# Performance work log

Hardware: AMD Instinct MI355X
Metric: run time of the kernel (lower is better)

The kernel has to match this reference:

```python
import jax, jax.numpy as jnp
import numpy as np

B, N, CIN, COUT = 16, 4096, 64, 128
M = N // 4          # number of FPS centroids
K = 64              # max_group_size
RADIUS = 0.2
EPS = 1e-5          # BatchNorm eps
BIG = 1e10


def fps(xyz, m):
    # xyz: [N,3] -> m farthest-point-sampled indices (first index = 0)
    n = xyz.shape[0]
    def step(carry, _):
        dists, last = carry
        d = jnp.sum((xyz - xyz[last]) ** 2, axis=-1)
        dists = jnp.minimum(dists, d)
        return (dists, jnp.argmax(dists).astype(jnp.int32)), last
    _, idx = jax.lax.scan(step, (jnp.full((n,), BIG, xyz.dtype), jnp.int32(0)), None, length=m)
    return idx


def ball_query(cent, xyz, radius, k):
    # cent: [M,3], xyz: [N,3] -> [M,K] indices; first-k-within-radius, padded with first hit
    n = xyz.shape[0]
    d2 = jnp.sum((cent[:, None, :] - xyz[None, :, :]) ** 2, axis=-1)  # [M,N]
    within = d2 <= radius * radius
    ar = jnp.arange(n, dtype=jnp.int32)
    key = jnp.where(within, ar, ar + n)         # in-radius points sort first, in index order
    order = jnp.argsort(key, axis=-1)[:, :k]    # first K candidates
    valid = jnp.take_along_axis(within, order, axis=-1)
    return jnp.where(valid, order, order[:, :1])


def conv1x1(x, w, b):
    # x: [B,C,K,M], w: [O,C] (Conv2d 1x1)
    return jnp.einsum('bckm,oc->bokm', x, w) + b[None, :, None, None]


def bnorm(x, g, b):
    # BatchNorm2d training-mode forward: stats over (B,K,M)
    mu = jnp.mean(x, axis=(0, 2, 3), keepdims=True)
    var = jnp.var(x, axis=(0, 2, 3), keepdims=True)
    return g[None, :, None, None] * (x - mu) * jax.lax.rsqrt(var + EPS) + b[None, :, None, None]


def setup_inputs() -> dict:
    key = jax.random.key(0)
    ks = jax.random.split(key, 6)
    def xavier(k, o, i):
        lim = float(np.sqrt(6.0 / (o + i)))
        return jax.random.uniform(k, (o, i), jnp.float32, -lim, lim)
    return {
        'points': jax.random.uniform(ks[0], (B, 3, N), jnp.float32),
        'point_features': jax.random.normal(ks[1], (B, CIN, N), jnp.float32),
        'w1': xavier(ks[2], CIN, CIN + 3), 'b1': jnp.zeros((CIN,), jnp.float32),
        'g1': jnp.ones((CIN,), jnp.float32), 'beta1': jnp.zeros((CIN,), jnp.float32),
        'w2': xavier(ks[3], CIN, CIN), 'b2': jnp.zeros((CIN,), jnp.float32),
        'g2': jnp.ones((CIN,), jnp.float32), 'beta2': jnp.zeros((CIN,), jnp.float32),
        'w3': xavier(ks[4], COUT, CIN), 'b3': jnp.zeros((COUT,), jnp.float32),
    }


def reference(points, point_features, w1, b1, g1, beta1, w2, b2, g2, beta2, w3, b3):
    xyz = jnp.transpose(points, (0, 2, 1))            # [B,N,3]
    feats = jnp.transpose(point_features, (0, 2, 1))  # [B,N,CIN]
    fps_idx = jax.vmap(lambda p: fps(p, M))(xyz)      # [B,M]
    cent = jax.vmap(lambda p, i: p[i])(xyz, fps_idx)  # [B,M,3]
    gidx = jax.vmap(lambda c, p: ball_query(c, p, RADIUS, K))(cent, xyz)  # [B,M,K]
    gxyz = jax.vmap(lambda p, i: p[i])(xyz, gidx) - cent[:, :, None, :]   # [B,M,K,3] relative coords
    gfeat = jax.vmap(lambda f, i: f[i])(feats, gidx)                      # [B,M,K,CIN]
    regions = jnp.concatenate([gxyz, gfeat], axis=-1)                     # [B,M,K,CIN+3]
    x = jnp.transpose(regions, (0, 3, 2, 1))                              # [B,CIN+3,K,M]
    x = jax.nn.relu(bnorm(conv1x1(x, w1, b1), g1, beta1))
    x = jax.nn.relu(bnorm(conv1x1(x, w2, b2), g2, beta2))
    x = conv1x1(x, w3, b3)
    centroid_features = jnp.max(x, axis=2)             # max over group dim -> [B,COUT,M]
    centroids = cent.reshape(B, 3, M)                  # faithful to original .view(B, 3, -1)
    return centroids, centroid_features
```

## Files before the change

kernel.cpp:

```cpp
#include <hip/hip_runtime.h>

#define NB   16
#define NPT  4096
#define CINF 64
#define COUTF 128
#define MC   1024
#define KG   64
#define PTOT (NB*KG*MC)

typedef unsigned short u16;
typedef unsigned int   u32;
typedef unsigned long long u64;

static __device__ __forceinline__ float blv(u16 v){ return __uint_as_float(((u32)v) << 16); }
static __device__ __forceinline__ u16 f2b(float f){
  u32 x = __float_as_uint(f);
  return (u16)((x + 0x7fffu + ((x >> 16) & 1u)) >> 16);
}

template<bool BF> struct io;
template<> struct io<true>{
  static __device__ __forceinline__ float ld(const void* p, size_t i){ return blv(((const u16*)p)[i]); }
  static __device__ __forceinline__ void st(void* p, size_t i, float v){ ((u16*)p)[i] = f2b(v); }
};
template<> struct io<false>{
  static __device__ __forceinline__ float ld(const void* p, size_t i){ return ((const float*)p)[i]; }
  static __device__ __forceinline__ void st(void* p, size_t i, float v){ ((float*)p)[i] = v; }
};

template<bool BF>
static __device__ __forceinline__ float4 ldw4(const void* w, int idx){
  if constexpr (BF) {
    ushort4 u = *(const ushort4*)((const u16*)w + idx);
    return make_float4(blv(u.x), blv(u.y), blv(u.z), blv(u.w));
  } else return *(const float4*)((const float*)w + idx);
}
template<bool BF>
static __device__ __forceinline__ void ldw8(const void* w, int idx, float4& a, float4& b){
  if constexpr (BF) {
    ushort4 u0 = *(const ushort4*)((const u16*)w + idx);
    ushort4 u1 = *(const ushort4*)((const u16*)w + idx + 4);
    a = make_float4(blv(u0.x), blv(u0.y), blv(u0.z), blv(u0.w));
    b = make_float4(blv(u1.x), blv(u1.y), blv(u1.z), blv(u1.w));
  } else {
    a = *(const float4*)((const float*)w + idx);
    b = *(const float4*)((const float*)w + idx + 4);
  }
}

__global__ __launch_bounds__(256) void detect_kernel(const void* pts, int* flagp, double* dstats)
{
  const int t = threadIdx.x;
  if (t < 64) {
    u32 w = ((const u32*)pts)[t];
    u64 m = __ballot((w & 0xFFFFu) < 0x4000u);
    if (t == 0) *flagp = (m == ~0ull) ? 1 : 0;
  }
  dstats[t] = 0.0;
}

template<bool BF>
static __device__ void fps_body(const void* pts, float* __restrict__ centw, void* out,
                                float* smp)
{
  float* lx = smp; float* ly = smp + NPT; float* lz = smp + 2*NPT;
  u64 (*red)[4] = (u64(*)[4])(smp + 3*NPT);
  const int t = threadIdx.x, b = blockIdx.x;
  const size_t pbase = (size_t)b*3*NPT;
  for (int i = t; i < NPT; i += 256) {
    lx[i] = io<BF>::ld(pts, pbase + i);
    ly[i] = io<BF>::ld(pts, pbase + NPT + i);
    lz[i] = io<BF>::ld(pts, pbase + 2*NPT + i);
  }
  __syncthreads();
  float qx[16],qy[16],qz[16],dd[16];
  const int base = t*16;
  #pragma unroll
  for (int j=0;j<16;++j){ qx[j]=lx[base+j]; qy[j]=ly[base+j]; qz[j]=lz[base+j]; dd[j]=1e10f; }
  int last = 0;
  const int lane = t & 63, wv = t >> 6;
  for (int it = 0; it < MC; ++it) {
    float cx = lx[last], cy = ly[last], cz = lz[last];
    if (t < 3) {
      float v = (t==0)?cx:((t==1)?cy:cz);
      centw[((size_t)b*MC + it)*3 + t] = v;
      io<BF>::st(out, (size_t)b*3*MC + (size_t)it*3 + t, v);
    }
    float bv = -1.f; int bi = base;
    #pragma unroll
    for (int j=0;j<16;++j) {
      float dx = __fsub_rn(qx[j], cx);
      float dy = __fsub_rn(qy[j], cy);
      float dz = __fsub_rn(qz[j], cz);
      float d  = __fadd_rn(__fadd_rn(__fmul_rn(dx,dx), __fmul_rn(dy,dy)), __fmul_rn(dz,dz));
      float nd = fminf(dd[j], d);
      dd[j] = nd;
      if (nd > bv) { bv = nd; bi = base + j; }
    }
    float mv = bv;
    #pragma unroll
    for (int off = 1; off < 64; off <<= 1) mv = fmaxf(mv, __shfl_xor(mv, off, 64));
    u64 wm = __ballot(bv == mv);
    int fl = __ffsll((long long)wm) - 1;
    int wbi = __shfl(bi, fl, 64);
    if (lane == 0) red[it & 1][wv] = ((u64)__float_as_uint(mv) << 32) | (u32)(~wbi);
    __syncthreads();
    u64 k0 = red[it&1][0], k1 = red[it&1][1];
    u64 k2 = red[it&1][2], k3 = red[it&1][3];
    if (k1 > k0) k0 = k1;
    if (k3 > k2) k2 = k3;
    if (k2 > k0) k0 = k2;
    last = (int)(~(u32)k0);
  }
}

template<bool BF>
static __device__ void g1_body(const void* pts, const void* feats, const void* w1p,
                               float* __restrict__ G1, float* smp)
{
  float* Xs = smp;
  void*  w1sh = (void*)(smp + 4352);
  const int idx = blockIdx.x - NB;
  const int b = idx >> 6;
  const int n0 = (idx & 63) * 64;
  const int t = threadIdx.x, lane = t & 63, wv = t >> 6;
  for (int e = t; e < 4352; e += 256) {
    int cp = e >> 6, co = e & 63;
    int src = (cp < 64) ? (co*67 + cp + 3) : (cp < 67 ? co*67 + cp - 64 : -1);
    if constexpr (BF) ((u16*)w1sh)[e]   = (src >= 0) ? ((const u16*)w1p)[src]   : (u16)0;
    else              ((float*)w1sh)[e] = (src >= 0) ? ((const float*)w1p)[src] : 0.f;
  }
  {
    float* xrow = Xs + lane*68;
    const size_t fb = ((size_t)b*CINF)*NPT + n0 + lane;
    #pragma unroll
    for (int j = 0; j < 16; ++j) {
      int c = wv*16 + j;
      xrow[c] = io<BF>::ld(feats, fb + (size_t)c*NPT);
    }
    if (wv == 0) {
      const size_t pb = (size_t)b*3*NPT + n0 + lane;
      xrow[64] = io<BF>::ld(pts, pb);
      xrow[65] = io<BF>::ld(pts, pb + NPT);
      xrow[66] = io<BF>::ld(pts, pb + 2*NPT);
      xrow[67] = 0.f;
    }
  }
  __syncthreads();
  const int kq = lane >> 4, coq = lane & 15;
  const int co0 = coq*4, k0 = wv*16 + kq*4;
  float acc[4][4];
  #pragma unroll
  for (int r=0;r<4;++r){
    #pragma unroll
    for (int j=0;j<4;++j) acc[r][j] = 0.f;
  }
  {
    const float* xb = Xs + (size_t)k0*68;
    for (int c4 = 0; c4 < 17; ++c4) {
      float4 xv[4], wr[4];
      #pragma unroll
      for (int r=0;r<4;++r) xv[r] = *(const float4*)(xb + r*68 + c4*4);
      #pragma unroll
      for (int q=0;q<4;++q) wr[q] = ldw4<BF>(w1sh, (c4*4+q)*64 + co0);
      #pragma unroll
      for (int q=0;q<4;++q){
        const float* w = (const float*)&wr[q];
        #pragma unroll
        for (int r=0;r<4;++r){
          const float x = ((const float*)&xv[r])[q];
          #pragma unroll
          for (int j=0;j<4;++j) acc[r][j] = fmaf(x, w[j], acc[r][j]);
        }
      }
    }
  }
  #pragma unroll
  for (int r=0;r<4;++r)
    *(float4*)(G1 + ((size_t)b*NPT + n0 + k0 + r)*64 + co0)
      = make_float4(acc[r][0],acc[r][1],acc[r][2],acc[r][3]);
}

__global__ __launch_bounds__(256) void fps_tr_kernel(const void* pts, const void* feats,
    const void* w1p, float* centw, float* G1, void* out, const int* flagp)
{
  __shared__ alignas(16) float smp[3*NPT + 16];
  if (blockIdx.x < NB) {
    if (*flagp) fps_body<true >(pts, centw, out, smp);
    else        fps_body<false>(pts, centw, out, smp);
  } else {
    if (*flagp) g1_body<true >(pts, feats, w1p, G1, smp);
    else        g1_body<false>(pts, feats, w1p, G1, smp);
  }
}

template<bool BF>
static __device__ void ballq_body(const void* pts, const float* __restrict__ centw,
                                  int* __restrict__ gidx)
{
  const int lane = threadIdx.x & 63;
  const int g = blockIdx.x*4 + (threadIdx.x >> 6);
  const int b = g >> 10;
  const size_t pbase = (size_t)b*3*NPT;
  const float cx = centw[(size_t)g*3+0], cy = centw[(size_t)g*3+1], cz = centw[(size_t)g*3+2];
  int* gout = gidx + (size_t)g*KG;
  int taken = 0, idx0 = 0;
  for (int s = 0; s < NPT; s += 64) {
    int n = s + lane;
    float dx = __fsub_rn(cx, io<BF>::ld(pts, pbase + n));
    float dy = __fsub_rn(cy, io<BF>::ld(pts, pbase + NPT + n));
    float dz = __fsub_rn(cz, io<BF>::ld(pts, pbase + 2*NPT + n));
    float d2 = __fadd_rn(__fadd_rn(__fmul_rn(dx,dx), __fmul_rn(dy,dy)), __fmul_rn(dz,dz));
    u64 mask = __ballot(d2 <= 0.04f);
    if (mask) {
      if (taken == 0) idx0 = s + __ffsll((long long)mask) - 1;
      bool win = (mask >> lane) & 1;
      int pos = taken + __popcll(mask & ((1ull << lane) - 1ull));
      if (win && pos < KG) gout[pos] = n;
      taken += (int)__popcll(mask);
      if (taken >= KG) break;
    }
  }
  int cnt = taken < KG ? taken : KG;
  if (lane >= cnt) gout[lane] = idx0;
}

__global__ __launch_bounds__(256) void ballq_kernel(const void* pts, const float* centw,
                                                    int* gidx, const int* flagp)
{
  if (*flagp) ballq_body<true >(pts, centw, gidx);
  else        ballq_body<false>(pts, centw, gidx);
}


template<bool BF>
__global__ __launch_bounds__(256) void p1_kernel(
    const void* w1p, const void* b1p,
    const float* __restrict__ centw, const int* __restrict__ gidxp,
    const float* __restrict__ G1,
    double* __restrict__ dstats, const int* __restrict__ flagp)
{
  if ((*flagp != 0) != BF) return;
  __shared__ int gids[64];
  __shared__ float d1s[64];
  __shared__ float w1cs[192];
  __shared__ float b1s[64];
  __shared__ float sbuf[128];
  const int t = threadIdx.x, lane = t & 63, cq = t >> 6;
  if (t < 64) {
    w1cs[t*3+0] = io<BF>::ld(w1p, (size_t)t*67 + 0);
    w1cs[t*3+1] = io<BF>::ld(w1p, (size_t)t*67 + 1);
    w1cs[t*3+2] = io<BF>::ld(w1p, (size_t)t*67 + 2);
    b1s[t] = io<BF>::ld(b1p, t);
  }
  const int g0 = blockIdx.x * 32;
  const int b = g0 >> 10;
  float s16[16], q16[16];
  #pragma unroll
  for (int j=0;j<16;++j){ s16[j]=0.f; q16[j]=0.f; }
  __syncthreads();
  for (int i = 0; i < 32; ++i) {
    const int g = g0 + i;
    if (t < 64) {
      gids[t] = gidxp[(size_t)g*KG + t];
      float cx = centw[(size_t)g*3], cy = centw[(size_t)g*3+1], cz = centw[(size_t)g*3+2];
      d1s[t] = b1s[t] - (w1cs[t*3]*cx + w1cs[t*3+1]*cy + w1cs[t*3+2]*cz);
    }
    __syncthreads();
    const float* row = G1 + ((size_t)b*NPT + gids[lane])*64 + cq*16;
    float vbuf[16];
    *(float4*)(vbuf)      = ((const float4*)row)[0];
    *(float4*)(vbuf + 4)  = ((const float4*)row)[1];
    *(float4*)(vbuf + 8)  = ((const float4*)row)[2];
    *(float4*)(vbuf + 12) = ((const float4*)row)[3];
    #pragma unroll
    for (int j=0;j<16;++j){
      float a = vbuf[j] + d1s[cq*16+j];
      s16[j] += a; q16[j] = fmaf(a, a, q16[j]);
    }
    __syncthreads();
  }
  #pragma unroll
  for (int j=0;j<16;++j){
    #pragma unroll
    for (int off = 1; off < 64; off <<= 1){
      s16[j] += __shfl_xor(s16[j], off, 64);
      q16[j] += __shfl_xor(q16[j], off, 64);
    }
  }
  if (lane == 0) {
    #pragma unroll
    for (int j=0;j<16;++j){ sbuf[cq*16+j] = s16[j]; sbuf[64+cq*16+j] = q16[j]; }
  }
  __syncthreads();
  if (t < 128) atomicAdd(&dstats[t], (double)sbuf[t]);
}

template<bool BF>
__global__ __launch_bounds__(256) void p2_kernel(
    const void* w1p, const void* b1p, const void* w2p, const void* b2p,
    const float* __restrict__ fstats, double* __restrict__ dstats,
    const float* __restrict__ centw, const int* __restrict__ gidxp,
    const float* __restrict__ G1, const int* __restrict__ flagp)
{
  if ((*flagp != 0) != BF) return;
  __shared__ alignas(16) float z1[2][4352];
  __shared__ alignas(16) unsigned char w2raw[BF ? 4096*2 : 4096*4];
  __shared__ float scsh[128];
  __shared__ int gids[128];
  __shared__ float c3s[6];

  const int t = threadIdx.x, lane = t & 63, wv = t >> 6;
  const int kq = lane >> 4, coq = lane & 15;
  const int co0 = coq * 4;
  const int k0  = wv*16 + kq*4;
  const int b   = blockIdx.x >> 7;
  const int m0  = (blockIdx.x & 127) * 8;
  const int c0  = (t*4) & 63;
  const int srow = t >> 4;

  for (int e = t; e < 4096; e += 256) {
    int src = (e & 63)*64 + (e >> 6);
    if constexpr (BF) ((u16*)w2raw)[e] = ((const u16*)w2p)[src];
    else              ((float*)w2raw)[e] = ((const float*)w2p)[src];
  }
  if (t < 128) scsh[t] = fstats[t];
  float b2v[4], w1c_r[12], b1_r[4];
  #pragma unroll
  for (int j=0;j<4;++j){
    b2v[j] = io<BF>::ld(b2p, co0+j);
    b1_r[j] = io<BF>::ld(b1p, c0+j);
    #pragma unroll
    for (int i=0;i<3;++i) w1c_r[j*3+i] = io<BF>::ld(w1p, (size_t)(c0+j)*67 + i);
  }
  __syncthreads();
  float scr[4], shr[4];
  #pragma unroll
  for (int j=0;j<4;++j){ scr[j] = scsh[c0+j]; shr[j] = scsh[64+c0+j]; }
  float sp[4] = {0,0,0,0}, qp[4] = {0,0,0,0};

  for (int mo = 0; mo < 4; ++mo) {
    const size_t g0 = (size_t)b*MC + m0 + mo*2;
    if (t < 128) gids[t] = gidxp[g0*KG + t];
    if (t < 6)   c3s[t]  = centw[g0*3 + t];
    __syncthreads();
    #pragma unroll
    for (int g=0;g<2;++g){
      float d1[4];
      {
        const float cx = c3s[g*3], cy = c3s[g*3+1], cz = c3s[g*3+2];
        #pragma unroll
        for (int j=0;j<4;++j)
          d1[j] = b1_r[j] - (w1c_r[j*3]*cx + w1c_r[j*3+1]*cy + w1c_r[j*3+2]*cz);
      }
      #pragma unroll
      for (int u=0;u<4;++u){
        const int row = u*16 + srow;
        const int gi = gids[g*64 + row];
        float4 v = *(const float4*)(G1 + ((size_t)b*NPT + gi)*64 + c0);
        float4 z;
        z.x = fmaxf(0.f, fmaf(v.x + d1[0], scr[0], shr[0]));
        z.y = fmaxf(0.f, fmaf(v.y + d1[1], scr[1], shr[1]));
        z.z = fmaxf(0.f, fmaf(v.z + d1[2], scr[2], shr[2]));
        z.w = fmaxf(0.f, fmaf(v.w + d1[3], scr[3], shr[3]));
        *(float4*)(z1[g] + (size_t)row*68 + c0) = z;
      }
    }
    __syncthreads();
    float acc[2][4][4];
    #pragma unroll
    for (int g=0;g<2;++g)
      #pragma unroll
      for (int r=0;r<4;++r)
        #pragma unroll
        for (int j=0;j<4;++j) acc[g][r][j] = b2v[j];
    {
      const float* zb0 = z1[0] + (size_t)k0*68;
      const float* zb1 = z1[1] + (size_t)k0*68;
      for (int c4 = 0; c4 < 16; ++c4) {
        float4 wr[4];
        #pragma unroll
        for (int q=0;q<4;++q) wr[q] = ldw4<BF>(w2raw, (c4*4+q)*64 + co0);
        float4 xv[2][4];
        #pragma unroll
        for (int r=0;r<4;++r){ xv[0][r] = *(const float4*)(zb0 + r*68 + c4*4);
                               xv[1][r] = *(const float4*)(zb1 + r*68 + c4*4); }
        #pragma unroll
        for (int q=0;q<4;++q){
          const float* w = (const float*)&wr[q];
          #pragma unroll
          for (int g=0;g<2;++g)
            #pragma unroll
            for (int r=0;r<4;++r){
              const float x = ((const float*)&xv[g][r])[q];
              #pragma unroll
              for (int j=0;j<4;++j) acc[g][r][j] = fmaf(x, w[j], acc[g][r][j]);
            }
        }
      }
    }
    #pragma unroll
    for (int g=0;g<2;++g){
      #pragma unroll
      for (int j=0;j<4;++j){
        sp[j] += (acc[g][0][j]+acc[g][1][j]) + (acc[g][2][j]+acc[g][3][j]);
        qp[j]  = fmaf(acc[g][0][j],acc[g][0][j], fmaf(acc[g][1][j],acc[g][1][j],
                 fmaf(acc[g][2][j],acc[g][2][j], fmaf(acc[g][3][j],acc[g][3][j], qp[j]))));
      }
    }
    __syncthreads();
  }
  float* sbuf = z1[0];
  #pragma unroll
  for (int j=0;j<4;++j){ sbuf[t*4+j] = sp[j]; sbuf[1024 + t*4+j] = qp[j]; }
  __syncthreads();
  if (t < 64) {
    const int cq = t >> 2, jj = t & 3;
    float s=0.f, q=0.f;
    #pragma unroll
    for (int i=0;i<16;++i){
      const int tp = cq + 16*i;
      s += sbuf[tp*4 + jj];
      q += sbuf[1024 + tp*4 + jj];
    }
    atomicAdd(&dstats[128 + t], (double)s);
    atomicAdd(&dstats[192 + t], (double)q);
  }
}

template<bool BF>
__global__ __launch_bounds__(256) void p3_kernel(
    const void* w1p, const void* b1p, const void* w2p, const void* b2p,
    const void* w3p, const void* b3p,
    const float* __restrict__ fstats,
    const float* __restrict__ centw, const int* __restrict__ gidxp,
    const float* __restrict__ G1, void* out, const int* __restrict__ flagp)
{
  if ((*flagp != 0) != BF) return;
  __shared__ alignas(16) float z[4352];
  __shared__ alignas(16) unsigned char w2raw[BF ? 4096*2 : 4096*4];
  __shared__ alignas(16) unsigned char w3raw[BF ? 8192*2 : 8192*4];
  __shared__ float scsh[256];
  __shared__ int gids[64];
  __shared__ float c3s[3];

  const int t = threadIdx.x, lane = t & 63, wv = t >> 6;
  const int kq = lane >> 4, coq = lane & 15;
  const int co0 = coq * 4;
  const int co08 = coq * 8;
  const int k0  = wv*16 + kq*4;
  const int b   = blockIdx.x >> 7;
  const int m0  = (blockIdx.x & 127) * 8;
  const int c0  = (t*4) & 63;
  const int srow = t >> 4;

  for (int e = t; e < 4096; e += 256) {
    int src = (e & 63)*64 + (e >> 6);
    if constexpr (BF) ((u16*)w2raw)[e] = ((const u16*)w2p)[src];
    else              ((float*)w2raw)[e] = ((const float*)w2p)[src];
  }
  for (int e = t; e < 8192; e += 256) {
    int src = (e & 127)*64 + (e >> 7);
    if constexpr (BF) ((u16*)w3raw)[e] = ((const u16*)w3p)[src];
    else              ((float*)w3raw)[e] = ((const float*)w3p)[src];
  }
  scsh[t] = fstats[t];
  float b2v[4], b3v[8], w1c_r[12], b1_r[4];
  #pragma unroll
  for (int j=0;j<4;++j){
    b2v[j] = io<BF>::ld(b2p, co0+j);
    b1_r[j] = io<BF>::ld(b1p, c0+j);
    #pragma unroll
    for (int i=0;i<3;++i) w1c_r[j*3+i] = io<BF>::ld(w1p, (size_t)(c0+j)*67 + i);
  }
  #pragma unroll
  for (int j=0;j<8;++j) b3v[j] = io<BF>::ld(b3p, co08+j);
  __syncthreads();
  float scr[4], shr[4], sc2[4], sh2[4];
  #pragma unroll
  for (int j=0;j<4;++j){
    scr[j] = scsh[c0+j];  shr[j] = scsh[64+c0+j];
    sc2[j] = scsh[128+co0+j]; sh2[j] = scsh[192+co0+j];
  }
  float outv[8];

  for (int mi = 0; mi < 8; ++mi) {
    const size_t g = (size_t)b*MC + m0 + mi;
    if (t < 64) gids[t] = gidxp[g*KG + t];
    if (t < 3)  c3s[t]  = centw[g*3 + t];
    __syncthreads();
    {
      float d1[4];
      const float cx = c3s[0], cy = c3s[1], cz = c3s[2];
      #pragma unroll
      for (int j=0;j<4;++j)
        d1[j] = b1_r[j] - (w1c_r[j*3]*cx + w1c_r[j*3+1]*cy + w1c_r[j*3+2]*cz);
      #pragma unroll
      for (int u=0;u<4;++u){
        const int row = u*16 + srow;
        const int gi = gids[row];
        float4 v = *(const float4*)(G1 + ((size_t)b*NPT + gi)*64 + c0);
        float4 zz;
        zz.x = fmaxf(0.f, fmaf(v.x + d1[0], scr[0], shr[0]));
        zz.y = fmaxf(0.f, fmaf(v.y + d1[1], scr[1], shr[1]));
        zz.z = fmaxf(0.f, fmaf(v.z + d1[2], scr[2], shr[2]));
        zz.w = fmaxf(0.f, fmaf(v.w + d1[3], scr[3], shr[3]));
        *(float4*)(z + (size_t)row*68 + c0) = zz;
      }
    }
    __syncthreads();
    float acc2[4][4];
    #pragma unroll
    for (int r=0;r<4;++r){
      #pragma unroll
      for (int j=0;j<4;++j) acc2[r][j] = b2v[j];
    }
    {
      const float* zb = z + (size_t)k0*68;
      for (int c4 = 0; c4 < 16; ++c4) {
        float4 xv[4], wr[4];
        #pragma unroll
        for (int r=0;r<4;++r) xv[r] = *(const float4*)(zb + r*68 + c4*4);
        #pragma unroll
        for (int q=0;q<4;++q) wr[q] = ldw4<BF>(w2raw, (c4*4+q)*64 + co0);
        #pragma unroll
        for (int q=0;q<4;++q){
          const float* w = (const float*)&wr[q];
          #pragma unroll
          for (int r=0;r<4;++r){
            const float x = ((const float*)&xv[r])[q];
            #pragma unroll
            for (int j=0;j<4;++j) acc2[r][j] = fmaf(x, w[j], acc2[r][j]);
          }
        }
      }
    }
    __syncthreads();
    #pragma unroll
    for (int r=0;r<4;++r){
      float4 zv;
      zv.x = fmaxf(0.f, fmaf(acc2[r][0], sc2[0], sh2[0]));
      zv.y = fmaxf(0.f, fmaf(acc2[r][1], sc2[1], sh2[1]));
      zv.z = fmaxf(0.f, fmaf(acc2[r][2], sc2[2], sh2[2]));
      zv.w = fmaxf(0.f, fmaf(acc2[r][3], sc2[3], sh2[3]));
      *(float4*)(z + (size_t)(k0+r)*68 + co0) = zv;
    }
    __syncthreads();
    float a3[4][8];
    #pragma unroll
    for (int r=0;r<4;++r){
      #pragma unroll
      for (int j=0;j<8;++j) a3[r][j] = b3v[j];
    }
    {
      const float* zb = z + (size_t)k0*68;
      for (int c4 = 0; c4 < 16; ++c4) {
        float4 xv[4], wr[4][2];
        #pragma unroll
        for (int r=0;r<4;++r) xv[r] = *(const float4*)(zb + r*68 + c4*4);
        #pragma unroll
        for (int q=0;q<4;++q) ldw8<BF>(w3raw, (c4*4+q)*128 + co08, wr[q][0], wr[q][1]);
        #pragma unroll
        for (int q=0;q<4;++q){
          const float* w = (const float*)&wr[q][0];
          #pragma unroll
          for (int r=0;r<4;++r){
            const float x = ((const float*)&xv[r])[q];
            #pragma unroll
            for (int j=0;j<8;++j) a3[r][j] = fmaf(x, w[j], a3[r][j]);
          }
        }
      }
    }
    __syncthreads();
    float* redm = z;
    #pragma unroll
    for (int j=0;j<8;++j){
      float mv = fmaxf(fmaxf(a3[0][j],a3[1][j]), fmaxf(a3[2][j],a3[3][j]));
      redm[(co08+j)*17 + wv*4 + kq] = mv;
    }
    __syncthreads();
    if (t < 128) {
      const float* rr = redm + t*17;
      float s = rr[0];
      #pragma unroll
      for (int i=1;i<16;++i) s = fmaxf(s, rr[i]);
      outv[mi] = s;
    }
    __syncthreads();
  }
  if (t < 128) {
    const size_t obase = (size_t)NB*3*MC + ((size_t)b*COUTF + t)*MC + m0;
    if (BF) {
      uint4 v;
      v.x = (u32)f2b(outv[0]) | ((u32)f2b(outv[1]) << 16);
      v.y = (u32)f2b(outv[2]) | ((u32)f2b(outv[3]) << 16);
      v.z = (u32)f2b(outv[4]) | ((u32)f2b(outv[5]) << 16);
      v.w = (u32)f2b(outv[6]) | ((u32)f2b(outv[7]) << 16);
      *(uint4*)((u16*)out + obase) = v;
    } else {
      float* op = (float*)out + obase;
      *(float4*)(op)     = make_float4(outv[0],outv[1],outv[2],outv[3]);
      *(float4*)(op + 4) = make_float4(outv[4],outv[5],outv[6],outv[7]);
    }
  }
}

template<int STAGE, bool BF>
__global__ __launch_bounds__(256) void mlp_kernel(
    const void* pts, const void* feats,
    const void* w1p, const void* b1p, const void* w2p, const void* b2p,
    const void* w3p, const void* b3p,
    const float* __restrict__ centw, const int* __restrict__ gidxp,
    double* __restrict__ dstats, const float* __restrict__ fstats, void* out,
    const int* __restrict__ flagp)
{
  if ((*flagp != 0) != BF) return;
  constexpr int ACTF = 4352 + (STAGE>=2 ? 4352 : 0);
  constexpr int W1B  = BF ? 4352*2 : 4352*4;
  constexpr int W2B  = (STAGE>=2) ? (BF ? 4096*2 : 4096*4) : 0;
  constexpr int W3B  = (STAGE==3) ? (BF ? 8192*2 : 8192*4) : 0;
  constexpr int REDB = (STAGE==1) ? 8704 : 0;
  constexpr int SMB  = ACTF*4 + W1B + W2B + W3B + REDB;
  __shared__ alignas(16) unsigned char smem[SMB];
  __shared__ int gids[64];
  __shared__ float c3s[3];
  float* Xs  = (float*)smem;
  float* z1s = Xs + 4352;
  void*  w1t = smem + ACTF*4;
  void*  w2t = smem + ACTF*4 + W1B;
  void*  w3t = smem + ACTF*4 + W1B + W2B;
  float* red = (STAGE==1) ? (float*)(smem + ACTF*4 + W1B) : z1s;
  const int t = threadIdx.x, lane = t & 63, wv = t >> 6;
  const int kq = lane >> 4, coq = lane & 15;
  const int co0 = coq * 4, co08 = coq * 8;
  const int k0  = wv*16 + kq*4;
  const int b   = blockIdx.x >> 7;
  const int m0  = (blockIdx.x & 127) * 8;
  for (int e = t; e < 4352; e += 256) {
    int cp = e >> 6, co = e & 63;
    int src = (cp < 64) ? (co*67 + cp + 3) : (cp < 67 ? co*67 + cp - 64 : -1);
    if constexpr (BF) ((u16*)w1t)[e]  = (src >= 0) ? ((const u16*)w1p)[src]  : (u16)0;
    else              ((float*)w1t)[e] = (src >= 0) ? ((const float*)w1p)[src] : 0.f;
  }
  if constexpr (STAGE >= 2)
    for (int e = t; e < 4096; e += 256) {
      int src = (e & 63)*64 + (e >> 6);
      if constexpr (BF) ((u16*)w2t)[e] = ((const u16*)w2p)[src];
      else              ((float*)w2t)[e] = ((const float*)w2p)[src];
    }
  if constexpr (STAGE == 3)
    for (int e = t; e < 8192; e += 256) {
      int src = (e & 127)*64 + (e >> 7);
      if constexpr (BF) ((u16*)w3t)[e] = ((const u16*)w3p)[src];
      else              ((float*)w3t)[e] = ((const float*)w3p)[src];
    }
  float b1v[4], b2v[4], sc1v[4], sh1v[4], sc2v[4], sh2v[4], b3v[8];
  #pragma unroll
  for (int j=0;j<4;++j) b1v[j] = io<BF>::ld(b1p, co0+j);
  if constexpr (STAGE >= 2) {
    #pragma unroll
    for (int j=0;j<4;++j) {
      b2v[j]  = io<BF>::ld(b2p, co0+j);
      sc1v[j] = fstats[co0+j]; sh1v[j] = fstats[64+co0+j];
    }
  }
  if constexpr (STAGE == 3) {
    #pragma unroll
    for (int j=0;j<4;++j) { sc2v[j] = fstats[128+co0+j]; sh2v[j] = fstats[192+co0+j]; }
    #pragma unroll
    for (int j=0;j<8;++j) b3v[j] = io<BF>::ld(b3p, co08+j);
  }
  float run_s = 0.f, run_q = 0.f;
  float outv[8];
  __syncthreads();
  for (int mi = 0; mi < 8; ++mi) {
    const int m = m0 + mi;
    const size_t g = (size_t)b*MC + m;
    if (t < 64) gids[t] = gidxp[g*KG + t];
    if (t < 3)  c3s[t]  = centw[g*3 + t];
    __syncthreads();
    {
      const int gi = gids[lane];
      float* xrow = Xs + lane*68;
      const int cs = wv*16;
      for (int c = cs; c < cs+16; ++c)
        xrow[c] = io<BF>::ld(feats, ((size_t)b*CINF + c)*NPT + gi);
      if (wv == 0) {
        const size_t pbase = (size_t)b*3*NPT;
        xrow[64] = __fsub_rn(io<BF>::ld(pts, pbase + gi),         c3s[0]);
        xrow[65] = __fsub_rn(io<BF>::ld(pts, pbase + NPT + gi),   c3s[1]);
        xrow[66] = __fsub_rn(io<BF>::ld(pts, pbase + 2*NPT + gi), c3s[2]);
        xrow[67] = 0.f;
      }
    }
    __syncthreads();
    float acc[4][4];
    #pragma unroll
    for (int r=0;r<4;++r){
      #pragma unroll
      for (int j=0;j<4;++j) acc[r][j] = b1v[j];
    }
    {
      const float* xb = Xs + (size_t)k0*68;
      for (int c4 = 0; c4 < 17; ++c4) {
        float4 xv[4], wr[4];
        #pragma unroll
        for (int r=0;r<4;++r) xv[r] = *(const float4*)(xb + r*68 + c4*4);
        #pragma unroll
        for (int q=0;q<4;++q) wr[q] = ldw4<BF>(w1t, (c4*4+q)*64 + co0);
        #pragma unroll
        for (int q=0;q<4;++q){
          const float* w = (const float*)&wr[q];
          #pragma unroll
          for (int r=0;r<4;++r){
            const float x = ((const float*)&xv[r])[q];
            #pragma unroll
            for (int j=0;j<4;++j) acc[r][j] = fmaf(x, w[j], acc[r][j]);
          }
        }
      }
    }
    if constexpr (STAGE == 1) {
      #pragma unroll
      for (int j=0;j<4;++j){
        float s  = (acc[0][j]+acc[1][j]) + (acc[2][j]+acc[3][j]);
        float q2 = fmaf(acc[0][j],acc[0][j], fmaf(acc[1][j],acc[1][j],
                   fmaf(acc[2][j],acc[2][j], acc[3][j]*acc[3][j])));
        red[(co0+j)*17 + wv*4 + kq] = s;
        red[1088 + (co0+j)*17 + wv*4 + kq] = q2;
      }
      __syncthreads();
      if (t < 64) {
        const float* r1 = red + t*17; const float* r2 = red + 1088 + t*17;
        float s=0.f, q=0.f;
        #pragma unroll
        for (int i=0;i<16;++i){ s += r1[i]; q += r2[i]; }
        run_s += s; run_q += q;
      }
    } else {
      #pragma unroll
      for (int r=0;r<4;++r){
        float4 zv;
        zv.x = fmaxf(0.f, fmaf(acc[r][0], sc1v[0], sh1v[0]));
        zv.y = fmaxf(0.f, fmaf(acc[r][1], sc1v[1], sh1v[1]));
        zv.z = fmaxf(0.f, fmaf(acc[r][2], sc1v[2], sh1v[2]));
        zv.w = fmaxf(0.f, fmaf(acc[r][3], sc1v[3], sh1v[3]));
        *(float4*)(z1s + (size_t)(k0+r)*68 + co0) = zv;
      }
      __syncthreads();
      float acc2[4][4];
      #pragma unroll
      for (int r=0;r<4;++r){
        #pragma unroll
        for (int j=0;j<4;++j) acc2[r][j] = b2v[j];
      }
      {
        const float* zb = z1s + (size_t)k0*68;
        for (int c4 = 0; c4 < 16; ++c4) {
          float4 xv[4], wr[4];
          #pragma unroll
          for (int r=0;r<4;++r) xv[r] = *(const float4*)(zb + r*68 + c4*4);
          #pragma unroll
          for (int q=0;q<4;++q) wr[q] = ldw4<BF>(w2t, (c4*4+q)*64 + co0);
          #pragma unroll
          for (int q=0;q<4;++q){
            const float* w = (const float*)&wr[q];
            #pragma unroll
            for (int r=0;r<4;++r){
              const float x = ((const float*)&xv[r])[q];
              #pragma unroll
              for (int j=0;j<4;++j) acc2[r][j] = fmaf(x, w[j], acc2[r][j]);
            }
          }
        }
      }
      if constexpr (STAGE == 2) {
        __syncthreads();
        #pragma unroll
        for (int j=0;j<4;++j){
          float s  = (acc2[0][j]+acc2[1][j]) + (acc2[2][j]+acc2[3][j]);
          float q2 = fmaf(acc2[0][j],acc2[0][j], fmaf(acc2[1][j],acc2[1][j],
                     fmaf(acc2[2][j],acc2[2][j], acc2[3][j]*acc2[3][j])));
          red[(co0+j)*17 + wv*4 + kq] = s;
          red[1088 + (co0+j)*17 + wv*4 + kq] = q2;
        }
        __syncthreads();
        if (t < 64) {
          const float* r1 = red + t*17; const float* r2 = red + 1088 + t*17;
          float s=0.f, q=0.f;
          #pragma unroll
          for (int i=0;i<16;++i){ s += r1[i]; q += r2[i]; }
          run_s += s; run_q += q;
        }
      } else {
        #pragma unroll
        for (int r=0;r<4;++r){
          float4 zv;
          zv.x = fmaxf(0.f, fmaf(acc2[r][0], sc2v[0], sh2v[0]));
          zv.y = fmaxf(0.f, fmaf(acc2[r][1], sc2v[1], sh2v[1]));
          zv.z = fmaxf(0.f, fmaf(acc2[r][2], sc2v[2], sh2v[2]));
          zv.w = fmaxf(0.f, fmaf(acc2[r][3], sc2v[3], sh2v[3]));
          *(float4*)(Xs + (size_t)(k0+r)*68 + co0) = zv;
        }
        __syncthreads();
        float a3[4][8];
        #pragma unroll
        for (int r=0;r<4;++r){
          #pragma unroll
          for (int j=0;j<8;++j) a3[r][j] = b3v[j];
        }
        {
          const float* zb = Xs + (size_t)k0*68;
          for (int c4 = 0; c4 < 16; ++c4) {
            float4 xv[4], wr[4][2];
            #pragma unroll
            for (int r=0;r<4;++r) xv[r] = *(const float4*)(zb + r*68 + c4*4);
            #pragma unroll
            for (int q=0;q<4;++q) ldw8<BF>(w3t, (c4*4+q)*128 + co08, wr[q][0], wr[q][1]);
            #pragma unroll
            for (int q=0;q<4;++q){
              const float* w = (const float*)&wr[q][0];
              #pragma unroll
              for (int r=0;r<4;++r){
                const float x = ((const float*)&xv[r])[q];
                #pragma unroll
                for (int j=0;j<8;++j) a3[r][j] = fmaf(x, w[j], a3[r][j]);
              }
            }
          }
        }
        float* redm = red;
        #pragma unroll
        for (int j=0;j<8;++j){
          float mv = fmaxf(fmaxf(a3[0][j],a3[1][j]), fmaxf(a3[2][j],a3[3][j]));
          redm[(co08+j)*17 + wv*4 + kq] = mv;
        }
        __syncthreads();
        if (t < 128) {
          const float* rr = redm + t*17;
          float s = rr[0];
          #pragma unroll
          for (int i=1;i<16;++i) s = fmaxf(s, rr[i]);
          outv[mi] = s;
        }
      }
    }
  }
  if constexpr (STAGE <= 2) {
    if (t < 64) {
      atomicAdd(&dstats[(STAGE==1 ? 0 : 128) + lane], (double)run_s);
      atomicAdd(&dstats[(STAGE==1 ? 64 : 192) + lane], (double)run_q);
    }
  } else {
    if (t < 128) {
      const size_t obase = (size_t)NB*3*MC + ((size_t)b*COUTF + t)*MC + m0;
      if (BF) {
        uint4 v;
        v.x = (u32)f2b(outv[0]) | ((u32)f2b(outv[1]) << 16);
        v.y = (u32)f2b(outv[2]) | ((u32)f2b(outv[3]) << 16);
        v.z = (u32)f2b(outv[4]) | ((u32)f2b(outv[5]) << 16);
        v.w = (u32)f2b(outv[6]) | ((u32)f2b(outv[7]) << 16);
        *(uint4*)((u16*)out + obase) = v;
      } else {
        float* op = (float*)out + obase;
        *(float4*)(op)     = make_float4(outv[0],outv[1],outv[2],outv[3]);
        *(float4*)(op + 4) = make_float4(outv[4],outv[5],outv[6],outv[7]);
      }
    }
  }
}

__global__ void finalize_kernel(const double* __restrict__ dstats, float* __restrict__ fstats,
                                const void* g, const void* beta, const int* flagp, int stage)
{
  const int t = threadIdx.x;
  const int off = (stage==1) ? 0 : 128;
  const double inv = 1.0 / (double)PTOT;
  double mu = dstats[off + t] * inv;
  double q  = dstats[off + 64 + t] * inv;
  double var = q - mu*mu;
  if (var < 0.0) var = 0.0;
  float gg, bb;
  if (*flagp) { gg = blv(((const u16*)g)[t]);  bb = blv(((const u16*)beta)[t]); }
  else        { gg = ((const float*)g)[t];     bb = ((const float*)beta)[t]; }
  double scale = (double)gg / sqrt(var + 1e-5);
  fstats[off + t]      = (float)scale;
  fstats[off + 64 + t] = bb - (float)(mu*scale);
}

extern "C" void kernel_launch(void* const* d_in, const int* in_sizes, int n_in,
                              void* d_out, int out_size, void* d_ws, size_t ws_size,
                              hipStream_t stream)
{
  (void)in_sizes; (void)n_in; (void)out_size;
  const void* pts  = d_in[0];
  const void* feats= d_in[1];
  const void* w1   = d_in[2];
  const void* b1   = d_in[3];
  const void* g1   = d_in[4];
  const void* be1  = d_in[5];
  const void* w2   = d_in[6];
  const void* b2   = d_in[7];
  const void* g2   = d_in[8];
  const void* be2  = d_in[9];
  const void* w3   = d_in[10];
  const void* b3   = d_in[11];

  char* ws = (char*)d_ws;
  int*    flag   = (int*)ws;
  double* dstats = (double*)(ws + 64);
  float*  fstats = (float*)(ws + 2112);
  float*  centw  = (float*)(ws + 4096);
  int*    gidx   = (int*)(ws + 200704);
  float*  G1     = (float*)(ws + 4395008);
  const bool gpath = ws_size >= 21172224ull;

  detect_kernel<<<1, 256, 0, stream>>>(pts, flag, dstats);
  fps_tr_kernel<<<gpath ? (NB + NB*NPT/64) : NB, 256, 0, stream>>>(pts, feats, w1, centw, G1, d_out, flag);
  ballq_kernel<<<NB*MC/4, 256, 0, stream>>>(pts, centw, gidx, flag);

  if (gpath) {
    p1_kernel<true ><<<NB*MC/32, 256, 0, stream>>>(w1, b1, centw, gidx, G1, dstats, flag);
    p1_kernel<false><<<NB*MC/32, 256, 0, stream>>>(w1, b1, centw, gidx, G1, dstats, flag);
    finalize_kernel<<<1, 64, 0, stream>>>(dstats, fstats, g1, be1, flag, 1);
    p2_kernel<true ><<<NB*MC/8, 256, 0, stream>>>(w1, b1, w2, b2, fstats, dstats, centw, gidx, G1, flag);
    p2_kernel<false><<<NB*MC/8, 256, 0, stream>>>(w1, b1, w2, b2, fstats, dstats, centw, gidx, G1, flag);
    finalize_kernel<<<1, 64, 0, stream>>>(dstats, fstats, g2, be2, flag, 2);
    p3_kernel<true ><<<NB*MC/8, 256, 0, stream>>>(w1, b1, w2, b2, w3, b3, fstats, centw, gidx, G1, d_out, flag);
    p3_kernel<false><<<NB*MC/8, 256, 0, stream>>>(w1, b1, w2, b2, w3, b3, fstats, centw, gidx, G1, d_out, flag);
  } else {
    const int GRID = NB*MC/8;
    mlp_kernel<1,true ><<<GRID, 256, 0, stream>>>(pts,feats,w1,b1,w2,b2,w3,b3,centw,gidx,dstats,fstats,d_out,flag);
    mlp_kernel<1,false><<<GRID, 256, 0, stream>>>(pts,feats,w1,b1,w2,b2,w3,b3,centw,gidx,dstats,fstats,d_out,flag);
    finalize_kernel<<<1, 64, 0, stream>>>(dstats, fstats, g1, be1, flag, 1);
    mlp_kernel<2,true ><<<GRID, 256, 0, stream>>>(pts,feats,w1,b1,w2,b2,w3,b3,centw,gidx,dstats,fstats,d_out,flag);
    mlp_kernel<2,false><<<GRID, 256, 0, stream>>>(pts,feats,w1,b1,w2,b2,w3,b3,centw,gidx,dstats,fstats,d_out,flag);
    finalize_kernel<<<1, 64, 0, stream>>>(dstats, fstats, g2, be2, flag, 2);
    mlp_kernel<3,true ><<<GRID, 256, 0, stream>>>(pts,feats,w1,b1,w2,b2,w3,b3,centw,gidx,dstats,fstats,d_out,flag);
    mlp_kernel<3,false><<<GRID, 256, 0, stream>>>(pts,feats,w1,b1,w2,b2,w3,b3,centw,gidx,dstats,fstats,d_out,flag);
  }
}
```

Before: 1.396 ms.

## Shorten FPS iteration critical path with DPP reduction and centroid coords in reduction

Replaces the shuffle-xor max reduction in farthest point sampling with DPP row operations plus a readlane, which should have lower latency. The winning point's coordinates now travel with the reduction key through shared memory, so the dependent shared-memory load of the next centroid is gone. Per-iteration global stores of centroids are buffered in LDS and written out once at the end. The cost is more shared memory, which could reduce occupancy for the co-scheduled G1 blocks that share this kernel.

```diff
diff --git a/kernel.cpp b/kernel.cpp
--- a/kernel.cpp
+++ b/kernel.cpp
@@ -48,6 +48,9 @@
   }
 }
 
+#define DPPMAXF(x, ctrl) \
+  (x) = fmaxf((x), __uint_as_float((u32)__builtin_amdgcn_update_dpp(0, (int)__float_as_uint(x), (ctrl), 0xF, 0xF, true)))
+
 __global__ __launch_bounds__(256) void detect_kernel(const void* pts, int* flagp, double* dstats)
 {
   const int t = threadIdx.x;
@@ -64,7 +67,9 @@
                                 float* smp)
 {
   float* lx = smp; float* ly = smp + NPT; float* lz = smp + 2*NPT;
-  u64 (*red)[4] = (u64(*)[4])(smp + 3*NPT);
+  float* cbuf = smp + 3*NPT;
+  u64*   rk   = (u64*)(smp + 3*NPT + 3072);
+  float4* rc  = (float4*)(smp + 3*NPT + 3072 + 16);
   const int t = threadIdx.x, b = blockIdx.x;
   const size_t pbase = (size_t)b*3*NPT;
   for (int i = t; i < NPT; i += 256) {
@@ -77,16 +82,12 @@
   const int base = t*16;
   #pragma unroll
   for (int j=0;j<16;++j){ qx[j]=lx[base+j]; qy[j]=ly[base+j]; qz[j]=lz[base+j]; dd[j]=1e10f; }
-  int last = 0;
   const int lane = t & 63, wv = t >> 6;
+  float cx = lx[0], cy = ly[0], cz = lz[0];
   for (int it = 0; it < MC; ++it) {
-    float cx = lx[last], cy = ly[last], cz = lz[last];
-    if (t < 3) {
-      float v = (t==0)?cx:((t==1)?cy:cz);
-      centw[((size_t)b*MC + it)*3 + t] = v;
-      io<BF>::st(out, (size_t)b*3*MC + (size_t)it*3 + t, v);
-    }
+    if (t == 0) { cbuf[it*3] = cx; cbuf[it*3+1] = cy; cbuf[it*3+2] = cz; }
     float bv = -1.f; int bi = base;
+    float bcx = qx[0], bcy = qy[0], bcz = qz[0];
     #pragma unroll
     for (int j=0;j<16;++j) {
       float dx = __fsub_rn(qx[j], cx);
@@ -95,22 +96,38 @@
       float d  = __fadd_rn(__fadd_rn(__fmul_rn(dx,dx), __fmul_rn(dy,dy)), __fmul_rn(dz,dz));
       float nd = fminf(dd[j], d);
       dd[j] = nd;
-      if (nd > bv) { bv = nd; bi = base + j; }
-    }
-    float mv = bv;
-    #pragma unroll
-    for (int off = 1; off < 64; off <<= 1) mv = fmaxf(mv, __shfl_xor(mv, off, 64));
+      if (nd > bv) { bv = nd; bi = base + j; bcx = qx[j]; bcy = qy[j]; bcz = qz[j]; }
+    }
+    float m = bv;
+    DPPMAXF(m, 0x111);
+    DPPMAXF(m, 0x112);
+    DPPMAXF(m, 0x114);
+    DPPMAXF(m, 0x118);
+    DPPMAXF(m, 0x142);
+    DPPMAXF(m, 0x143);
+    const float mv = __uint_as_float((u32)__builtin_amdgcn_readlane((int)__float_as_uint(m), 63));
     u64 wm = __ballot(bv == mv);
     int fl = __ffsll((long long)wm) - 1;
-    int wbi = __shfl(bi, fl, 64);
-    if (lane == 0) red[it & 1][wv] = ((u64)__float_as_uint(mv) << 32) | (u32)(~wbi);
-    __syncthreads();
-    u64 k0 = red[it&1][0], k1 = red[it&1][1];
-    u64 k2 = red[it&1][2], k3 = red[it&1][3];
-    if (k1 > k0) k0 = k1;
-    if (k3 > k2) k2 = k3;
-    if (k2 > k0) k0 = k2;
-    last = (int)(~(u32)k0);
+    const int p = it & 1;
+    if (lane == fl) {
+      rk[p*4 + wv] = ((u64)__float_as_uint(mv) << 32) | (u32)(~bi);
+      rc[p*4 + wv] = make_float4(bcx, bcy, bcz, 0.f);
+    }
+    __syncthreads();
+    u64 ka = rk[p*4+0], kb = rk[p*4+1], kc2 = rk[p*4+2], kd = rk[p*4+3];
+    float4 c0 = rc[p*4+0], c1 = rc[p*4+1], c2 = rc[p*4+2], c3 = rc[p*4+3];
+    bool s01 = kb > ka;  u64 k01 = s01 ? kb : ka;
+    bool s23 = kd > kc2; u64 k23 = s23 ? kd : kc2;
+    float cwx = s01 ? c1.x : c0.x, cwy = s01 ? c1.y : c0.y, cwz = s01 ? c1.z : c0.z;
+    float cvx = s23 ? c3.x : c2.x, cvy = s23 ? c3.y : c2.y, cvz = s23 ? c3.z : c2.z;
+    bool sx = k23 > k01;
+    cx = sx ? cvx : cwx; cy = sx ? cvy : cwy; cz = sx ? cvz : cwz;
+  }
+  __syncthreads();
+  for (int i = t; i < 3*MC; i += 256) {
+    float v = cbuf[i];
+    centw[(size_t)b*3*MC + i] = v;
+    io<BF>::st(out, (size_t)b*3*MC + i, v);
   }
 }
 
@@ -184,7 +201,7 @@
 __global__ __launch_bounds__(256) void fps_tr_kernel(const void* pts, const void* feats,
     const void* w1p, float* centw, float* G1, void* out, const int* flagp)
 {
-  __shared__ alignas(16) float smp[3*NPT + 16];
+  __shared__ alignas(16) float smp[15408];
   if (blockIdx.x < NB) {
     if (*flagp) fps_body<true >(pts, centw, out, smp);
     else        fps_body<false>(pts, centw, out, smp);
```

Result: slower. 1.497 ms (+7.3%).

## Restructure p3 kernel to per-wave groups with larger register tiles

Applied to the files above, without the earlier changes.

Rewrites the final MLP stage so that each wavefront independently processes its own centroid group in a private shared-memory slice. Each thread now computes an 8x8 (conv2) and 8x16 (conv3) register tile instead of 4x4/4x8, and block-wide __syncthreads are removed from the inner loop. The grid is cut to 512 blocks that handle 32 groups each, and the max reduction is done per wave with direct scattered output stores. This aims to cut barrier overhead and raise arithmetic intensity per LDS load. In exchange it uses much more register pressure and LDS (launch_bounds 256,1), which may reduce occupancy, and the output writes are less coalesced.

```diff
diff --git a/kernel.cpp b/kernel.cpp
--- a/kernel.cpp
+++ b/kernel.cpp
@@ -429,7 +429,7 @@
 }
 
 template<bool BF>
-__global__ __launch_bounds__(256) void p3_kernel(
+__global__ __launch_bounds__(256, 1) void p3_kernel(
     const void* w1p, const void* b1p, const void* w2p, const void* b2p,
     const void* w3p, const void* b3p,
     const float* __restrict__ fstats,
@@ -437,22 +437,17 @@
     const float* __restrict__ G1, void* out, const int* __restrict__ flagp)
 {
   if ((*flagp != 0) != BF) return;
-  __shared__ alignas(16) float z[4352];
+  __shared__ alignas(16) float z[4][4352];
   __shared__ alignas(16) unsigned char w2raw[BF ? 4096*2 : 4096*4];
   __shared__ alignas(16) unsigned char w3raw[BF ? 8192*2 : 8192*4];
-  __shared__ float scsh[256];
-  __shared__ int gids[64];
-  __shared__ float c3s[3];
+  __shared__ alignas(16) float scsh[256];
+  __shared__ alignas(16) float w1cs[192];
+  __shared__ alignas(16) float b1s[64];
+  __shared__ alignas(16) float d1b[4][64];
+  __shared__ alignas(16) float pm[4][1056];
 
   const int t = threadIdx.x, lane = t & 63, wv = t >> 6;
-  const int kq = lane >> 4, coq = lane & 15;
-  const int co0 = coq * 4;
-  const int co08 = coq * 8;
-  const int k0  = wv*16 + kq*4;
-  const int b   = blockIdx.x >> 7;
-  const int m0  = (blockIdx.x & 127) * 8;
-  const int c0  = (t*4) & 63;
-  const int srow = t >> 4;
+  const int lr = lane >> 3, lc = lane & 7;
 
   for (int e = t; e < 4096; e += 256) {
     int src = (e & 63)*64 + (e >> 6);
@@ -465,143 +460,156 @@
     else              ((float*)w3raw)[e] = ((const float*)w3p)[src];
   }
   scsh[t] = fstats[t];
-  float b2v[4], b3v[8], w1c_r[12], b1_r[4];
-  #pragma unroll
-  for (int j=0;j<4;++j){
-    b2v[j] = io<BF>::ld(b2p, co0+j);
-    b1_r[j] = io<BF>::ld(b1p, c0+j);
-    #pragma unroll
-    for (int i=0;i<3;++i) w1c_r[j*3+i] = io<BF>::ld(w1p, (size_t)(c0+j)*67 + i);
-  }
-  #pragma unroll
-  for (int j=0;j<8;++j) b3v[j] = io<BF>::ld(b3p, co08+j);
+  if (t < 64) {
+    w1cs[t*3+0] = io<BF>::ld(w1p, (size_t)t*67 + 0);
+    w1cs[t*3+1] = io<BF>::ld(w1p, (size_t)t*67 + 1);
+    w1cs[t*3+2] = io<BF>::ld(w1p, (size_t)t*67 + 2);
+    b1s[t] = io<BF>::ld(b1p, t);
+  }
+  float b2v[8], b3v[16], sc2r[8], sh2r[8];
+  #pragma unroll
+  for (int j=0;j<8;++j)  b2v[j] = io<BF>::ld(b2p, lc*8 + j);
+  #pragma unroll
+  for (int j=0;j<16;++j) b3v[j] = io<BF>::ld(b3p, lc*16 + j);
   __syncthreads();
-  float scr[4], shr[4], sc2[4], sh2[4];
-  #pragma unroll
-  for (int j=0;j<4;++j){
-    scr[j] = scsh[c0+j];  shr[j] = scsh[64+c0+j];
-    sc2[j] = scsh[128+co0+j]; sh2[j] = scsh[192+co0+j];
-  }
-  float outv[8];
-
-  for (int mi = 0; mi < 8; ++mi) {
-    const size_t g = (size_t)b*MC + m0 + mi;
-    if (t < 64) gids[t] = gidxp[g*KG + t];
-    if (t < 3)  c3s[t]  = centw[g*3 + t];
-    __syncthreads();
+  #pragma unroll
+  for (int j=0;j<8;++j){ sc2r[j] = scsh[128 + lc*8 + j]; sh2r[j] = scsh[192 + lc*8 + j]; }
+
+  float* zw = z[wv];
+  float* pmw = pm[wv];
+
+  for (int gi_it = 0; gi_it < 8; ++gi_it) {
+    const int g = blockIdx.x*32 + wv*8 + gi_it;
+    const int b = g >> 10, m = g & (MC-1);
     {
-      float d1[4];
-      const float cx = c3s[0], cy = c3s[1], cz = c3s[2];
-      #pragma unroll
-      for (int j=0;j<4;++j)
-        d1[j] = b1_r[j] - (w1c_r[j*3]*cx + w1c_r[j*3+1]*cy + w1c_r[j*3+2]*cz);
-      #pragma unroll
-      for (int u=0;u<4;++u){
-        const int row = u*16 + srow;
-        const int gi = gids[row];
-        float4 v = *(const float4*)(G1 + ((size_t)b*NPT + gi)*64 + c0);
+      const float cx = centw[(size_t)g*3], cy = centw[(size_t)g*3+1], cz = centw[(size_t)g*3+2];
+      d1b[wv][lane] = b1s[lane] - (w1cs[lane*3]*cx + w1cs[lane*3+1]*cy + w1cs[lane*3+2]*cz);
+    }
+    {
+      const int gi = gidxp[(size_t)g*KG + lane];
+      const float* grow = G1 + ((size_t)b*NPT + gi)*64;
+      float* zrow = zw + (size_t)lane*68;
+      #pragma unroll
+      for (int c0 = 0; c0 < 64; c0 += 4) {
+        float4 gv = *(const float4*)(grow + c0);
+        float4 dv = *(const float4*)(&d1b[wv][c0]);
+        float4 s1 = *(const float4*)(&scsh[c0]);
+        float4 h1 = *(const float4*)(&scsh[64 + c0]);
         float4 zz;
-        zz.x = fmaxf(0.f, fmaf(v.x + d1[0], scr[0], shr[0]));
-        zz.y = fmaxf(0.f, fmaf(v.y + d1[1], scr[1], shr[1]));
-        zz.z = fmaxf(0.f, fmaf(v.z + d1[2], scr[2], shr[2]));
-        zz.w = fmaxf(0.f, fmaf(v.w + d1[3], scr[3], shr[3]));
-        *(float4*)(z + (size_t)row*68 + c0) = zz;
-      }
-    }
-    __syncthreads();
-    float acc2[4][4];
-    #pragma unroll
-    for (int r=0;r<4;++r){
-      #pragma unroll
-      for (int j=0;j<4;++j) acc2[r][j] = b2v[j];
-    }
+        zz.x = fmaxf(0.f, fmaf(gv.x + dv.x, s1.x, h1.x));
+        zz.y = fmaxf(0.f, fmaf(gv.y + dv.y, s1.y, h1.y));
+        zz.z = fmaxf(0.f, fmaf(gv.z + dv.z, s1.z, h1.z));
+        zz.w = fmaxf(0.f, fmaf(gv.w + dv.w, s1.w, h1.w));
+        *(float4*)(zrow + c0) = zz;
+      }
+    }
+    float acc[8][8];
+    #pragma unroll
+    for (int r=0;r<8;++r)
+      #pragma unroll
+      for (int j=0;j<8;++j) acc[r][j] = b2v[j];
     {
-      const float* zb = z + (size_t)k0*68;
+      const float* zb = zw + (size_t)(lr*8)*68;
       for (int c4 = 0; c4 < 16; ++c4) {
-        float4 xv[4], wr[4];
-        #pragma unroll
-        for (int r=0;r<4;++r) xv[r] = *(const float4*)(zb + r*68 + c4*4);
-        #pragma unroll
-        for (int q=0;q<4;++q) wr[q] = ldw4<BF>(w2raw, (c4*4+q)*64 + co0);
+        float4 xv[8], wA[4], wB[4];
+        #pragma unroll
+        for (int r=0;r<8;++r) xv[r] = *(const float4*)(zb + r*68 + c4*4);
+        #pragma unroll
+        for (int q=0;q<4;++q) ldw8<BF>(w2raw, (c4*4+q)*64 + lc*8, wA[q], wB[q]);
         #pragma unroll
         for (int q=0;q<4;++q){
-          const float* w = (const float*)&wr[q];
-          #pragma unroll
-          for (int r=0;r<4;++r){
+          const float* wa = (const float*)&wA[q];
+          const float* wb = (const float*)&wB[q];
+          #pragma unroll
+          for (int r=0;r<8;++r){
             const float x = ((const float*)&xv[r])[q];
             #pragma unroll
-            for (int j=0;j<4;++j) acc2[r][j] = fmaf(x, w[j], acc2[r][j]);
+            for (int j=0;j<4;++j){
+              acc[r][j]   = fmaf(x, wa[j], acc[r][j]);
+              acc[r][4+j] = fmaf(x, wb[j], acc[r][4+j]);
+            }
           }
         }
       }
     }
-    __syncthreads();
-    #pragma unroll
-    for (int r=0;r<4;++r){
-      float4 zv;
-      zv.x = fmaxf(0.f, fmaf(acc2[r][0], sc2[0], sh2[0]));
-      zv.y = fmaxf(0.f, fmaf(acc2[r][1], sc2[1], sh2[1]));
-      zv.z = fmaxf(0.f, fmaf(acc2[r][2], sc2[2], sh2[2]));
-      zv.w = fmaxf(0.f, fmaf(acc2[r][3], sc2[3], sh2[3]));
-      *(float4*)(z + (size_t)(k0+r)*68 + co0) = zv;
-    }
-    __syncthreads();
-    float a3[4][8];
-    #pragma unroll
-    for (int r=0;r<4;++r){
-      #pragma unroll
-      for (int j=0;j<8;++j) a3[r][j] = b3v[j];
-    }
+    #pragma unroll
+    for (int r=0;r<8;++r){
+      float4 v0, v1;
+      v0.x = fmaxf(0.f, fmaf(acc[r][0], sc2r[0], sh2r[0]));
+      v0.y = fmaxf(0.f, fmaf(acc[r][1], sc2r[1], sh2r[1]));
+      v0.z = fmaxf(0.f, fmaf(acc[r][2], sc2r[2], sh2r[2]));
+      v0.w = fmaxf(0.f, fmaf(acc[r][3], sc2r[3], sh2r[3]));
+      v1.x = fmaxf(0.f, fmaf(acc[r][4], sc2r[4], sh2r[4]));
+      v1.y = fmaxf(0.f, fmaf(acc[r][5], sc2r[5], sh2r[5]));
+      v1.z = fmaxf(0.f, fmaf(acc[r][6], sc2r[6], sh2r[6]));
+      v1.w = fmaxf(0.f, fmaf(acc[r][7], sc2r[7], sh2r[7]));
+      *(float4*)(zw + (size_t)(lr*8+r)*68 + lc*8)     = v0;
+      *(float4*)(zw + (size_t)(lr*8+r)*68 + lc*8 + 4) = v1;
+    }
+    float a3[8][16];
+    #pragma unroll
+    for (int r=0;r<8;++r)
+      #pragma unroll
+      for (int j=0;j<16;++j) a3[r][j] = b3v[j];
     {
-      const float* zb = z + (size_t)k0*68;
+      const float* zb = zw + (size_t)(lr*8)*68;
       for (int c4 = 0; c4 < 16; ++c4) {
-        float4 xv[4], wr[4][2];
-        #pragma unroll
-        for (int r=0;r<4;++r) xv[r] = *(const float4*)(zb + r*68 + c4*4);
-        #pragma unroll
-        for (int q=0;q<4;++q) ldw8<BF>(w3raw, (c4*4+q)*128 + co08, wr[q][0], wr[q][1]);
+        float4 xv[8], w0[4], w1v[4], w2v[4], w3v[4];
+        #pragma unroll
+        for (int r=0;r<8;++r) xv[r] = *(const float4*)(zb + r*68 + c4*4);
         #pragma unroll
         for (int q=0;q<4;++q){
-          const float* w = (const float*)&wr[q][0];
-          #pragma unroll
-          for (int r=0;r<4;++r){
+          w0[q]  = ldw4<BF>(w3raw, (c4*4+q)*128 + lc*16);
+          w1v[q] = ldw4<BF>(w3raw, (c4*4+q)*128 + lc*16 + 4);
+          w2v[q] = ldw4<BF>(w3raw, (c4*4+q)*128 + lc*16 + 8);
+          w3v[q] = ldw4<BF>(w3raw, (c4*4+q)*128 + lc*16 + 12);
+        }
+        #pragma unroll
+        for (int q=0;q<4;++q){
+          const float* wa = (const float*)&w0[q];
+          const float* wb = (const float*)&w1v[q];
+          const float* wc = (const float*)&w2v[q];
+          const float* wd = (const float*)&w3v[q];
+          #pragma unroll
+          for (int r=0;r<8;++r){
             const float x = ((const float*)&xv[r])[q];
             #pragma unroll
-            for (int j=0;j<8;++j) a3[r][j] = fmaf(x, w[j], a3[r][j]);
+            for (int j=0;j<4;++j){
+              a3[r][j]    = fmaf(x, wa[j], a3[r][j]);
+              a3[r][4+j]  = fmaf(x, wb[j], a3[r][4+j]);
+              a3[r][8+j]  = fmaf(x, wc[j], a3[r][8+j]);
+              a3[r][12+j] = fmaf(x, wd[j], a3[r][12+j]);
+            }
           }
         }
       }
     }
-    __syncthreads();
-    float* redm = z;
-    #pragma unroll
-    for (int j=0;j<8;++j){
-      float mv = fmaxf(fmaxf(a3[0][j],a3[1][j]), fmaxf(a3[2][j],a3[3][j]));
-      redm[(co08+j)*17 + wv*4 + kq] = mv;
-    }
-    __syncthreads();
-    if (t < 128) {
-      const float* rr = redm + t*17;
-      float s = rr[0];
-      #pragma unroll
-      for (int i=1;i<16;++i) s = fmaxf(s, rr[i]);
-      outv[mi] = s;
-    }
-    __syncthreads();
-  }
-  if (t < 128) {
-    const size_t obase = (size_t)NB*3*MC + ((size_t)b*COUTF + t)*MC + m0;
-    if (BF) {
-      uint4 v;
-      v.x = (u32)f2b(outv[0]) | ((u32)f2b(outv[1]) << 16);
-      v.y = (u32)f2b(outv[2]) | ((u32)f2b(outv[3]) << 16);
-      v.z = (u32)f2b(outv[4]) | ((u32)f2b(outv[5]) << 16);
-      v.w = (u32)f2b(outv[6]) | ((u32)f2b(outv[7]) << 16);
-      *(uint4*)((u16*)out + obase) = v;
-    } else {
-      float* op = (float*)out + obase;
-      *(float4*)(op)     = make_float4(outv[0],outv[1],outv[2],outv[3]);
-      *(float4*)(op + 4) = make_float4(outv[4],outv[5],outv[6],outv[7]);
+    {
+      float mx[16];
+      #pragma unroll
+      for (int j=0;j<16;++j){
+        float v = a3[0][j];
+        #pragma unroll
+        for (int r=1;r<8;++r) v = fmaxf(v, a3[r][j]);
+        mx[j] = v;
+      }
+      float* pr = pmw + (size_t)lr*132 + lc*16;
+      *(float4*)(pr)      = make_float4(mx[0], mx[1], mx[2], mx[3]);
+      *(float4*)(pr + 4)  = make_float4(mx[4], mx[5], mx[6], mx[7]);
+      *(float4*)(pr + 8)  = make_float4(mx[8], mx[9], mx[10], mx[11]);
+      *(float4*)(pr + 12) = make_float4(mx[12], mx[13], mx[14], mx[15]);
+    }
+    {
+      #pragma unroll
+      for (int cc = 0; cc < 2; ++cc) {
+        const int co = lane*2 + cc;
+        float v = pmw[co];
+        #pragma unroll
+        for (int r=1;r<8;++r) v = fmaxf(v, pmw[(size_t)r*132 + co]);
+        const size_t oidx = (size_t)NB*3*MC + ((size_t)b*COUTF + co)*MC + m;
+        if (BF) ((u16*)out)[oidx] = f2b(v);
+        else    ((float*)out)[oidx] = v;
+      }
     }
   }
 }
@@ -927,8 +935,8 @@
     p2_kernel<true ><<<NB*MC/8, 256, 0, stream>>>(w1, b1, w2, b2, fstats, dstats, centw, gidx, G1, flag);
     p2_kernel<false><<<NB*MC/8, 256, 0, stream>>>(w1, b1, w2, b2, fstats, dstats, centw, gidx, G1, flag);
     finalize_kernel<<<1, 64, 0, stream>>>(dstats, fstats, g2, be2, flag, 2);
-    p3_kernel<true ><<<NB*MC/8, 256, 0, stream>>>(w1, b1, w2, b2, w3, b3, fstats, centw, gidx, G1, d_out, flag);
-    p3_kernel<false><<<NB*MC/8, 256, 0, stream>>>(w1, b1, w2, b2, w3, b3, fstats, centw, gidx, G1, d_out, flag);
+    p3_kernel<true ><<<512, 256, 0, stream>>>(w1, b1, w2, b2, w3, b3, fstats, centw, gidx, G1, d_out, flag);
+    p3_kernel<false><<<512, 256, 0, stream>>>(w1, b1, w2, b2, w3, b3, fstats, centw, gidx, G1, d_out, flag);
   } else {
     const int GRID = NB*MC/8;
     mlp_kernel<1,true ><<<GRID, 256, 0, stream>>>(pts,feats,w1,b1,w2,b2,w3,b3,centw,gidx,dstats,fstats,d_out,flag);
```

After: 1.403 ms. Within noise of the previous version (+0.5%).
